# Kernel optimization log

Hardware: AMD Instinct MI355X
Metric: run time of the kernel (lower is better)

Reference implementation:

```python
import jax, jax.numpy as jnp
import numpy as np


def setup_inputs() -> dict:
    key = jax.random.key(0)
    k1, k2, k3 = jax.random.split(key, 3)
    B, C, E, L, W = 4, 2, 256, 16000, 40
    mixture_w = jax.random.normal(k1, (B, E, L), dtype=jnp.float32)
    est_mask = jax.random.uniform(k2, (B, C, E, L), dtype=jnp.float32)
    basis_w = jax.random.normal(k3, (W, E), dtype=jnp.float32) * (1.0 / np.sqrt(E))
    return {"mixture_w": mixture_w, "est_mask": est_mask, "basis_w": basis_w}


def overlap_and_add(frames, frame_step):
    # frames: [B, C, L, W] -> [B, C, T] with T = (L-1)*frame_step + W
    B, C, L, W = frames.shape
    T = (L - 1) * frame_step + W
    # scatter-add each frame into the output waveform at its strided offset
    idx = (jnp.arange(L)[:, None] * frame_step + jnp.arange(W)[None, :]).reshape(-1)
    out = jnp.zeros((B, C, T), dtype=frames.dtype)
    return out.at[..., idx].add(frames.reshape(B, C, L * W))


def reference(mixture_w, est_mask, basis_w):
    # mixture_w: [B, E, L], est_mask: [B, C, E, L], basis_w: [W, E]
    source_w = mixture_w[:, None, :, :] * est_mask          # [B, C, E, L]
    # transpose(2,3) then Linear(E->W): contract over E
    est_frames = jnp.einsum('bcel,we->bclw', source_w, basis_w)  # [B, C, L, W]
    W = basis_w.shape[0]
    return overlap_and_add(est_frames, W // 2)              # [B, C, T]
```

## Files before the change

### kernel.cpp

```cpp
#include <hip/hip_runtime.h>
#include <hip/hip_bf16.h>

#define BQ   4
#define CQ   2
#define EQ   256
#define LQ   16000
#define WQ   40
#define STEP 20
#define TQ   ((LQ - 1) * STEP + WQ)
#define TLF  127
#define OWN  (TLF * STEP)
#define NBX  126

__global__ __launch_bounds__(256) void decoder_kernel(
    const float* __restrict__ mix,
    const float* __restrict__ mask,
    const float* __restrict__ basis,
    float* __restrict__ out)
{
    __shared__ __align__(16) float basisT[EQ * WQ];
    __shared__ float outS[CQ][TLF * STEP + WQ + STEP];

    const int tid = threadIdx.x;
    const int c   = tid >> 7;
    const int ll  = tid & 127;
    const int bx  = blockIdx.x;
    const int b   = blockIdx.y;
    const int f   = TLF * bx - 1 + ll;

    for (int i = tid; i < EQ * WQ; i += 256) {
        int w = i >> 8;
        int e = i & (EQ - 1);
        basisT[e * WQ + w] = basis[i];
    }
    if (tid < CQ * STEP) {
        int cc = tid / STEP;
        int i  = tid % STEP;
        outS[cc][TLF * STEP + STEP + i] = 0.0f;
    }
    __syncthreads();

    float acc[WQ];
#pragma unroll
    for (int w = 0; w < WQ; ++w) acc[w] = 0.0f;

    if (f >= 0 && f < LQ) {
        const float* mp = mix  + (size_t)b * EQ * LQ + f;
        const float* kp = mask + (size_t)(b * CQ + c) * EQ * LQ + f;
#pragma unroll 2
        for (int e = 0; e < EQ; ++e) {
            float m = *mp;
            float k = *kp;
            mp += LQ;
            kp += LQ;
            float s = m * k;
            const float4* bt = (const float4*)(&basisT[e * WQ]);
#pragma unroll
            for (int j = 0; j < WQ / 4; ++j) {
                float4 bv = bt[j];
                acc[4 * j + 0] = fmaf(s, bv.x, acc[4 * j + 0]);
                acc[4 * j + 1] = fmaf(s, bv.y, acc[4 * j + 1]);
                acc[4 * j + 2] = fmaf(s, bv.z, acc[4 * j + 2]);
                acc[4 * j + 3] = fmaf(s, bv.w, acc[4 * j + 3]);
            }
        }
    }

    const int base = ll * STEP;
    if ((ll & 1) == 0) {
#pragma unroll
        for (int w = 0; w < WQ; ++w) outS[c][base + w] = acc[w];
    }
    __syncthreads();
    if (ll & 1) {
#pragma unroll
        for (int w = 0; w < WQ; ++w) outS[c][base + w] += acc[w];
    }
    __syncthreads();

    for (int cc = 0; cc < CQ; ++cc) {
        const size_t ob = ((size_t)b * CQ + cc) * TQ + (size_t)OWN * bx;
        for (int i = tid; i < OWN; i += 256) {
            const long t = (long)OWN * bx + i;
            if (t < (long)TQ) {
                out[ob + i] = outS[cc][STEP + i];
            }
        }
    }
}

extern "C" void kernel_launch(void* const* d_in, const int* in_sizes, int n_in,
                              void* d_out, int out_size, void* d_ws, size_t ws_size,
                              hipStream_t stream) {
    const float* mix   = (const float*)d_in[0];
    const float* mask  = (const float*)d_in[1];
    const float* basis = (const float*)d_in[2];
    float* out = (float*)d_out;

    dim3 grid(NBX, BQ);
    decoder_kernel<<<grid, 256, 0, stream>>>(mix, mask, basis, out);
}
```

Before: 278.7 us.

## Split embedding reduction across two thread halves per block and batch loads

Doubles the block to 512 threads, with each half reducing over half of the E dimension. Partial frame sums are merged through shared memory in four serialized phases. The inner loop now issues four mix and mask loads before computing, to raise memory-level parallelism. The aim is more waves in flight for a latency-bound kernel with only 504 blocks, at the cost of extra barriers and shared-memory accumulation passes.

Measured after the change: 243.1 us. 12.8% less time.

```diff
diff --git a/kernel.cpp b/kernel.cpp
--- a/kernel.cpp
+++ b/kernel.cpp
@@ -11,8 +11,9 @@
 #define TLF  127
 #define OWN  (TLF * STEP)
 #define NBX  126
+#define EH   (EQ / 2)
 
-__global__ __launch_bounds__(256) void decoder_kernel(
+__global__ __launch_bounds__(512, 4) void decoder_kernel(
     const float* __restrict__ mix,
     const float* __restrict__ mask,
     const float* __restrict__ basis,
@@ -22,13 +23,14 @@
     __shared__ float outS[CQ][TLF * STEP + WQ + STEP];
 
     const int tid = threadIdx.x;
-    const int c   = tid >> 7;
     const int ll  = tid & 127;
+    const int c   = (tid >> 7) & 1;
+    const int h   = tid >> 8;
     const int bx  = blockIdx.x;
     const int b   = blockIdx.y;
     const int f   = TLF * bx - 1 + ll;
 
-    for (int i = tid; i < EQ * WQ; i += 256) {
+    for (int i = tid; i < EQ * WQ; i += 512) {
         int w = i >> 8;
         int e = i & (EQ - 1);
         basisT[e * WQ + w] = basis[i];
@@ -45,34 +47,49 @@
     for (int w = 0; w < WQ; ++w) acc[w] = 0.0f;
 
     if (f >= 0 && f < LQ) {
-        const float* mp = mix  + (size_t)b * EQ * LQ + f;
-        const float* kp = mask + (size_t)(b * CQ + c) * EQ * LQ + f;
-#pragma unroll 2
-        for (int e = 0; e < EQ; ++e) {
-            float m = *mp;
-            float k = *kp;
-            mp += LQ;
-            kp += LQ;
-            float s = m * k;
-            const float4* bt = (const float4*)(&basisT[e * WQ]);
+        const float* mp = mix  + ((size_t)b * EQ + h * EH) * LQ + f;
+        const float* kp = mask + (((size_t)(b * CQ + c)) * EQ + h * EH) * LQ + f;
+        const float* bt0 = &basisT[(h * EH) * WQ];
+        for (int eo = 0; eo < EH; eo += 4) {
+            float m[4], k[4];
 #pragma unroll
-            for (int j = 0; j < WQ / 4; ++j) {
-                float4 bv = bt[j];
-                acc[4 * j + 0] = fmaf(s, bv.x, acc[4 * j + 0]);
-                acc[4 * j + 1] = fmaf(s, bv.y, acc[4 * j + 1]);
-                acc[4 * j + 2] = fmaf(s, bv.z, acc[4 * j + 2]);
-                acc[4 * j + 3] = fmaf(s, bv.w, acc[4 * j + 3]);
+            for (int u = 0; u < 4; ++u) {
+                m[u] = mp[(size_t)(eo + u) * LQ];
+                k[u] = kp[(size_t)(eo + u) * LQ];
+            }
+#pragma unroll
+            for (int u = 0; u < 4; ++u) {
+                float s = m[u] * k[u];
+                const float4* bt = (const float4*)(bt0 + (eo + u) * WQ);
+#pragma unroll
+                for (int j = 0; j < WQ / 4; ++j) {
+                    float4 bv = bt[j];
+                    acc[4 * j + 0] = fmaf(s, bv.x, acc[4 * j + 0]);
+                    acc[4 * j + 1] = fmaf(s, bv.y, acc[4 * j + 1]);
+                    acc[4 * j + 2] = fmaf(s, bv.z, acc[4 * j + 2]);
+                    acc[4 * j + 3] = fmaf(s, bv.w, acc[4 * j + 3]);
+                }
             }
         }
     }
 
     const int base = ll * STEP;
-    if ((ll & 1) == 0) {
+    if (h == 0 && (ll & 1) == 0) {
 #pragma unroll
         for (int w = 0; w < WQ; ++w) outS[c][base + w] = acc[w];
     }
     __syncthreads();
-    if (ll & 1) {
+    if (h == 0 && (ll & 1)) {
+#pragma unroll
+        for (int w = 0; w < WQ; ++w) outS[c][base + w] += acc[w];
+    }
+    __syncthreads();
+    if (h == 1 && (ll & 1) == 0) {
+#pragma unroll
+        for (int w = 0; w < WQ; ++w) outS[c][base + w] += acc[w];
+    }
+    __syncthreads();
+    if (h == 1 && (ll & 1)) {
 #pragma unroll
         for (int w = 0; w < WQ; ++w) outS[c][base + w] += acc[w];
     }
@@ -80,7 +97,7 @@
 
     for (int cc = 0; cc < CQ; ++cc) {
         const size_t ob = ((size_t)b * CQ + cc) * TQ + (size_t)OWN * bx;
-        for (int i = tid; i < OWN; i += 256) {
+        for (int i = tid; i < OWN; i += 512) {
             const long t = (long)OWN * bx + i;
             if (t < (long)TQ) {
                 out[ob + i] = outS[cc][STEP + i];
@@ -98,5 +115,5 @@
     float* out = (float*)d_out;
 
     dim3 grid(NBX, BQ);
-    decoder_kernel<<<grid, 256, 0, stream>>>(mix, mask, basis, out);
+    decoder_kernel<<<grid, 512, 0, stream>>>(mix, mask, basis, out);
 }
```

## Split E reduction across four wave groups and read pre-transposed basis from global

Applied to the files above, without the earlier changes.

Moves the basis transpose into a separate small kernel that writes to workspace, so each block no longer rebuilds a 40KB shared copy. Each block now covers 63 frames with 512 threads, and the E dimension is split into four quarters whose partial accumulators are merged through two shared output buffers with staged syncs. The intent is more blocks and waves for latency hiding and a lower per-block setup and shared-memory footprint. In exchange the basis is read via wave-uniform global/scalar loads, there are extra barriers and shared-memory reduction traffic, and halo frames are recomputed more often.

Result: faster. 242.7 us (-12.9%).

```diff
diff --git a/kernel.cpp b/kernel.cpp
--- a/kernel.cpp
+++ b/kernel.cpp
@@ -1,5 +1,4 @@
 #include <hip/hip_runtime.h>
-#include <hip/hip_bf16.h>
 
 #define BQ   4
 #define CQ   2
@@ -8,82 +7,99 @@
 #define WQ   40
 #define STEP 20
 #define TQ   ((LQ - 1) * STEP + WQ)
-#define TLF  127
+#define TLF  63
 #define OWN  (TLF * STEP)
-#define NBX  126
+#define NBX  254
+#define NH   4
+#define EH   (EQ / NH)
+#define SPAN (TLF * STEP + WQ + STEP)
 
-__global__ __launch_bounds__(256) void decoder_kernel(
+__global__ void transpose_basis_kernel(const float* __restrict__ basis,
+                                       float* __restrict__ wsT) {
+    int i = blockIdx.x * 256 + threadIdx.x;
+    if (i < EQ * WQ) {
+        int e = i / WQ;
+        int w = i - e * WQ;
+        wsT[i] = basis[w * EQ + e];
+    }
+}
+
+__global__ __launch_bounds__(512, 8) void decoder_kernel(
     const float* __restrict__ mix,
     const float* __restrict__ mask,
-    const float* __restrict__ basis,
+    const float* __restrict__ wsT,
     float* __restrict__ out)
 {
-    __shared__ __align__(16) float basisT[EQ * WQ];
-    __shared__ float outS[CQ][TLF * STEP + WQ + STEP];
+    __shared__ float outS[2][CQ][SPAN];
 
     const int tid = threadIdx.x;
-    const int c   = tid >> 7;
-    const int ll  = tid & 127;
+    const int ll  = tid & 63;
+    const int c   = (tid >> 6) & 1;
+    const int h   = __builtin_amdgcn_readfirstlane(tid >> 7);
     const int bx  = blockIdx.x;
     const int b   = blockIdx.y;
     const int f   = TLF * bx - 1 + ll;
 
-    for (int i = tid; i < EQ * WQ; i += 256) {
-        int w = i >> 8;
-        int e = i & (EQ - 1);
-        basisT[e * WQ + w] = basis[i];
-    }
-    if (tid < CQ * STEP) {
-        int cc = tid / STEP;
-        int i  = tid % STEP;
-        outS[cc][TLF * STEP + STEP + i] = 0.0f;
-    }
-    __syncthreads();
+    const int   fc    = min(max(f, 0), LQ - 1);
+    const float valid = (f >= 0 && f < LQ) ? 1.0f : 0.0f;
 
     float acc[WQ];
 #pragma unroll
     for (int w = 0; w < WQ; ++w) acc[w] = 0.0f;
 
-    if (f >= 0 && f < LQ) {
-        const float* mp = mix  + (size_t)b * EQ * LQ + f;
-        const float* kp = mask + (size_t)(b * CQ + c) * EQ * LQ + f;
-#pragma unroll 2
-        for (int e = 0; e < EQ; ++e) {
-            float m = *mp;
-            float k = *kp;
-            mp += LQ;
-            kp += LQ;
-            float s = m * k;
-            const float4* bt = (const float4*)(&basisT[e * WQ]);
+    const float* mp = mix  + ((size_t)b * EQ + h * EH) * LQ + fc;
+    const float* kp = mask + (((size_t)(b * CQ + c)) * EQ + h * EH) * LQ + fc;
+    const float* bp = wsT + (size_t)h * EH * WQ;
+
+    for (int eo = 0; eo < EH; eo += 2) {
+        float m0 = mp[(size_t)eo * LQ];
+        float m1 = mp[(size_t)(eo + 1) * LQ];
+        float k0 = kp[(size_t)eo * LQ] * valid;
+        float k1 = kp[(size_t)(eo + 1) * LQ] * valid;
+        {
+            float s = m0 * k0;
+            const float* bb = bp + eo * WQ;
 #pragma unroll
-            for (int j = 0; j < WQ / 4; ++j) {
-                float4 bv = bt[j];
-                acc[4 * j + 0] = fmaf(s, bv.x, acc[4 * j + 0]);
-                acc[4 * j + 1] = fmaf(s, bv.y, acc[4 * j + 1]);
-                acc[4 * j + 2] = fmaf(s, bv.z, acc[4 * j + 2]);
-                acc[4 * j + 3] = fmaf(s, bv.w, acc[4 * j + 3]);
-            }
+            for (int w = 0; w < WQ; ++w) acc[w] = fmaf(s, bb[w], acc[w]);
+        }
+        {
+            float s = m1 * k1;
+            const float* bb = bp + (eo + 1) * WQ;
+#pragma unroll
+            for (int w = 0; w < WQ; ++w) acc[w] = fmaf(s, bb[w], acc[w]);
         }
     }
 
     const int base = ll * STEP;
-    if ((ll & 1) == 0) {
+    const int cp   = h >> 1;
+    const int hp   = h & 1;
+    if (hp == 0 && (ll & 1) == 0) {
 #pragma unroll
-        for (int w = 0; w < WQ; ++w) outS[c][base + w] = acc[w];
+        for (int w = 0; w < WQ; ++w) outS[cp][c][base + w] = acc[w];
     }
     __syncthreads();
-    if (ll & 1) {
+    if (hp == 0 && (ll & 1) == 1) {
 #pragma unroll
-        for (int w = 0; w < WQ; ++w) outS[c][base + w] += acc[w];
+        for (int w = 0; w < WQ; ++w) outS[cp][c][base + w] += acc[w];
+    }
+    __syncthreads();
+    if (hp == 1 && (ll & 1) == 0) {
+#pragma unroll
+        for (int w = 0; w < WQ; ++w) outS[cp][c][base + w] += acc[w];
+    }
+    __syncthreads();
+    if (hp == 1 && (ll & 1) == 1) {
+#pragma unroll
+        for (int w = 0; w < WQ; ++w) outS[cp][c][base + w] += acc[w];
     }
     __syncthreads();
 
     for (int cc = 0; cc < CQ; ++cc) {
         const size_t ob = ((size_t)b * CQ + cc) * TQ + (size_t)OWN * bx;
-        for (int i = tid; i < OWN; i += 256) {
+        for (int i = tid; i < OWN; i += 512) {
             const long t = (long)OWN * bx + i;
             if (t < (long)TQ) {
-                out[ob + i] = outS[cc][STEP + i];
+                out[ob + i] = outS[0][cc][STEP + i] + outS[1][cc][STEP + i];
             }
         }
     }
@@ -96,7 +112,10 @@
     const float* mask  = (const float*)d_in[1];
     const float* basis = (const float*)d_in[2];
     float* out = (float*)d_out;
+    float* wsT = (float*)d_ws;
+
+    transpose_basis_kernel<<<dim3((EQ * WQ + 255) / 256), 256, 0, stream>>>(basis, wsT);
 
     dim3 grid(NBX, BQ);
-    decoder_kernel<<<grid, 256, 0, stream>>>(mix, mask, basis, out);
+    decoder_kernel<<<grid, 512, 0, stream>>>(mix, mask, wsT, out);
 }
```
